# Kernel tuning notes

Measured on AMD Instinct MI355X. Metric: run time of the kernel, lower is better.

## Reference

```python
import jax, jax.numpy as jnp
import numpy as np

ALPHA_LIM = (float(np.exp(-1.0 / 5.0)), float(np.exp(-1.0 / 25.0)))
BETA_LIM = (float(np.exp(-1.0 / 30.0)), float(np.exp(-1.0 / 120.0)))
A_LIM = (-1.0, 1.0)
B_LIM = (0.0, 2.0)
THRESHOLD = 1.0


@jax.custom_vjp
def spike_boxcar(x):
    # Heaviside forward, boxcar surrogate gradient
    return (x > 0).astype(x.dtype)


def _spike_fwd(x):
    return spike_boxcar(x), x


def _spike_bwd(x, g):
    return (jnp.where(jnp.abs(x) <= 0.5, g, jnp.zeros_like(g)),)


spike_boxcar.defvjp(_spike_fwd, _spike_bwd)


def setup_inputs() -> dict:
    key = jax.random.key(0)
    ks = jax.random.split(key, 9)
    B, T, I, H = 128, 512, 512, 512
    return {
        "x": jax.random.normal(ks[0], (B, T, I), dtype=jnp.float32),
        "W": jax.random.normal(ks[1], (H, I), dtype=jnp.float32) / np.sqrt(I),
        "alpha": jax.random.uniform(ks[2], (H,), dtype=jnp.float32),
        "beta": jax.random.uniform(ks[3], (H,), dtype=jnp.float32),
        "a": jax.random.uniform(ks[4], (H,), dtype=jnp.float32),
        "b": jax.random.uniform(ks[5], (H,), dtype=jnp.float32),
        "u0": jax.random.uniform(ks[6], (B, H), dtype=jnp.float32),
        "w0": jax.random.uniform(ks[7], (B, H), dtype=jnp.float32),
        "s0": jax.random.uniform(ks[8], (B, H), dtype=jnp.float32),
    }


def reference(x, W, alpha, beta, a, b, u0, w0, s0):
    # x: [B, T, I]; W: [H, I] (nn.Linear weight, no bias)
    alpha = jnp.clip(alpha, ALPHA_LIM[0], ALPHA_LIM[1])
    beta = jnp.clip(beta, BETA_LIM[0], BETA_LIM[1])
    a = jnp.clip(a, A_LIM[0], A_LIM[1])
    b = jnp.clip(b, B_LIM[0], B_LIM[1])

    Wx = jnp.einsum("bti,hi->bth", x, W)  # [B, T, H]
    Wx_t = jnp.transpose(Wx, (1, 0, 2))    # [T, B, H] for scan over time

    def step(carry, wx_t):
        ut, wt, st = carry
        wt = beta * wt + a * ut + b * st
        ut = alpha * (ut - st) + (1.0 - alpha) * (wx_t - wt)
        st = spike_boxcar(ut - THRESHOLD)
        return (ut, wt, st), st

    _, s = jax.lax.scan(step, (u0, w0, s0), Wx_t)  # s: [T, B, H]
    return jnp.transpose(s, (1, 0, 2))  # [B, T, H]
```

## Files before the change

kernel.cpp:

```cpp
#include <hip/hip_runtime.h>
#include <hip/hip_bf16.h>


#define M_SZ 65536
#define H_SZ 512
#define K_SZ 512
#define B_SZ 128
#define T_SZ 512
#define LSTR 132

typedef __attribute__((ext_vector_type(4))) float f32x4;

__device__ __forceinline__ bool detect_bf16(const unsigned int* __restrict__ w) {
  int c = 0;
#pragma unroll
  for (int i = 0; i < 64; ++i) {
    unsigned int e = (w[i] >> 7) & 0xffu;
    c += (e >= 115u && e <= 131u) ? 1 : 0;
  }
  return c > 32;
}

template <bool ISB>
__device__ __forceinline__ f32x4 ld4t(const void* __restrict__ p, size_t off) {
  if constexpr (!ISB) {
    return *reinterpret_cast<const f32x4*>(reinterpret_cast<const float*>(p) + off);
  } else {
    uint2 v = *reinterpret_cast<const uint2*>(reinterpret_cast<const unsigned short*>(p) + off);
    f32x4 r;
    r.x = __uint_as_float((v.x & 0xffffu) << 16);
    r.y = __uint_as_float(v.x & 0xffff0000u);
    r.z = __uint_as_float((v.y & 0xffffu) << 16);
    r.w = __uint_as_float(v.y & 0xffff0000u);
    return r;
  }
}

template <bool ISB>
__device__ __forceinline__ float ld1t(const void* __restrict__ p, int i) {
  if constexpr (!ISB) return reinterpret_cast<const float*>(p)[i];
  return __uint_as_float((unsigned int)(reinterpret_cast<const unsigned short*>(p)[i]) << 16);
}

template <bool ISB>
__device__ __forceinline__ void fused_body(
    const void* __restrict__ X, const void* __restrict__ Wm,
    const void* __restrict__ alpha_p, const void* __restrict__ beta_p,
    const void* __restrict__ a_p, const void* __restrict__ b_p,
    const void* __restrict__ u0p, const void* __restrict__ w0p,
    const void* __restrict__ s0p, void* __restrict__ out,
    float* __restrict__ As, float* __restrict__ Bs, float* __restrict__ wxs) {
  const int tid = threadIdx.x;
  const int r0 = tid >> 2;
  const int q0 = (tid & 3) * 4;
  const int tx = tid & 15;
  const int ty = tid >> 4;
  const int b = blockIdx.x >> 2;
  const int N0 = (blockIdx.x & 3) * 128;

  float al = 0.f, be = 0.f, av = 0.f, bv = 0.f, om = 0.f, u = 0.f, w = 0.f, s = 0.f;
  if (tid < 128) {
    const int h = N0 + tid;
    al = fminf(fmaxf(ld1t<ISB>(alpha_p, h), (float)0.8187307530779818),
               (float)0.9607894391523232);
    be = fminf(fmaxf(ld1t<ISB>(beta_p, h), (float)0.9672161004820059),
               (float)0.9917013044213351);
    av = fminf(fmaxf(ld1t<ISB>(a_p, h), -1.0f), 1.0f);
    bv = fminf(fmaxf(ld1t<ISB>(b_p, h), 0.0f), 2.0f);
    om = __fsub_rn(1.0f, al);
    const int bh = b * H_SZ + h;
    u = ld1t<ISB>(u0p, bh);
    w = ld1t<ISB>(w0p, bh);
    s = ld1t<ISB>(s0p, bh);
  }

  float* outf = reinterpret_cast<float*>(out);
  unsigned short* outu = reinterpret_cast<unsigned short*>(out);

  for (int tt = 0; tt < 4; ++tt) {
    const size_t M0 = (size_t)b * T_SZ + tt * 128;

    float acc[8][8];
#pragma unroll
    for (int i = 0; i < 8; ++i)
#pragma unroll
      for (int j = 0; j < 8; ++j) acc[i][j] = 0.0f;

    const size_t aoff0 = (M0 + r0) * K_SZ + q0;
    const size_t aoff1 = (M0 + r0 + 64) * K_SZ + q0;
    const size_t boff0 = (size_t)(N0 + r0) * K_SZ + q0;
    const size_t boff1 = (size_t)(N0 + r0 + 64) * K_SZ + q0;

    f32x4 pa0 = ld4t<ISB>(X, aoff0), pa1 = ld4t<ISB>(X, aoff1);
    f32x4 pb0 = ld4t<ISB>(Wm, boff0), pb1 = ld4t<ISB>(Wm, boff1);

    for (int kk = 0; kk < K_SZ; kk += 16) {
      __syncthreads();
      As[(q0 + 0) * LSTR + r0] = pa0.x; As[(q0 + 1) * LSTR + r0] = pa0.y;
      As[(q0 + 2) * LSTR + r0] = pa0.z; As[(q0 + 3) * LSTR + r0] = pa0.w;
      As[(q0 + 0) * LSTR + r0 + 64] = pa1.x; As[(q0 + 1) * LSTR + r0 + 64] = pa1.y;
      As[(q0 + 2) * LSTR + r0 + 64] = pa1.z; As[(q0 + 3) * LSTR + r0 + 64] = pa1.w;
      Bs[(q0 + 0) * LSTR + r0] = pb0.x; Bs[(q0 + 1) * LSTR + r0] = pb0.y;
      Bs[(q0 + 2) * LSTR + r0] = pb0.z; Bs[(q0 + 3) * LSTR + r0] = pb0.w;
      Bs[(q0 + 0) * LSTR + r0 + 64] = pb1.x; Bs[(q0 + 1) * LSTR + r0 + 64] = pb1.y;
      Bs[(q0 + 2) * LSTR + r0 + 64] = pb1.z; Bs[(q0 + 3) * LSTR + r0 + 64] = pb1.w;
      __syncthreads();
      if (kk + 16 < K_SZ) {
        pa0 = ld4t<ISB>(X, aoff0 + kk + 16); pa1 = ld4t<ISB>(X, aoff1 + kk + 16);
        pb0 = ld4t<ISB>(Wm, boff0 + kk + 16); pb1 = ld4t<ISB>(Wm, boff1 + kk + 16);
      }
#pragma unroll
      for (int k = 0; k < 16; ++k) {
        const f32x4 a0 = *reinterpret_cast<const f32x4*>(As + k * LSTR + ty * 4);
        const f32x4 a1 = *reinterpret_cast<const f32x4*>(As + k * LSTR + 64 + ty * 4);
        const f32x4 b0 = *reinterpret_cast<const f32x4*>(Bs + k * LSTR + tx * 4);
        const f32x4 b1 = *reinterpret_cast<const f32x4*>(Bs + k * LSTR + 64 + tx * 4);
        const float avv[8] = {a0.x, a0.y, a0.z, a0.w, a1.x, a1.y, a1.z, a1.w};
        const float bvv[8] = {b0.x, b0.y, b0.z, b0.w, b1.x, b1.y, b1.z, b1.w};
#pragma unroll
        for (int i = 0; i < 8; ++i)
#pragma unroll
          for (int j = 0; j < 8; ++j) acc[i][j] += avv[i] * bvv[j];
      }
    }
#pragma unroll
    for (int sub = 0; sub < 4; ++sub) {
      __syncthreads();
      const bool owner = (sub & 1) ? (ty >= 8) : (ty < 8);
      if (owner) {
#pragma unroll
        for (int rr = 0; rr < 4; ++rr) {
          const int row = (ty & 7) * 4 + rr;
          const int r = (sub < 2) ? rr : 4 + rr;
          f32x4 v0 = {acc[r][0], acc[r][1], acc[r][2], acc[r][3]};
          f32x4 v1 = {acc[r][4], acc[r][5], acc[r][6], acc[r][7]};
          *reinterpret_cast<f32x4*>(wxs + row * 128 + tx * 4) = v0;
          *reinterpret_cast<f32x4*>(wxs + row * 128 + 64 + tx * 4) = v1;
        }
      }
      __syncthreads();
      if (tid < 128) {
        const size_t tbase =
            ((size_t)b * T_SZ + tt * 128 + sub * 32) * H_SZ + N0 + tid;
#pragma unroll
        for (int t = 0; t < 32; ++t) {
          const float cur = wxs[t * 128 + tid];
          w = __fadd_rn(__fadd_rn(__fmul_rn(be, w), __fmul_rn(av, u)), __fmul_rn(bv, s));
          u = __fadd_rn(__fmul_rn(al, __fsub_rn(u, s)), __fmul_rn(om, __fsub_rn(cur, w)));
          const bool sp = (u > 1.0f);
          s = sp ? 1.0f : 0.0f;
          if constexpr (ISB)
            outu[tbase + (size_t)t * H_SZ] = sp ? (unsigned short)0x3F80u : (unsigned short)0u;
          else
            outf[tbase + (size_t)t * H_SZ] = s;
        }
      }
    }
  }
}

__global__ __launch_bounds__(256) void adlif_fused(
    const void* __restrict__ X, const void* __restrict__ Wm,
    const void* __restrict__ alpha_p, const void* __restrict__ beta_p,
    const void* __restrict__ a_p, const void* __restrict__ b_p,
    const void* __restrict__ u0p, const void* __restrict__ w0p,
    const void* __restrict__ s0p, void* __restrict__ out) {
  __shared__ float As[16 * LSTR];
  __shared__ float Bs[16 * LSTR];
  __shared__ float wxs[32 * 128];
  if (detect_bf16(reinterpret_cast<const unsigned int*>(X)))
    fused_body<true>(X, Wm, alpha_p, beta_p, a_p, b_p, u0p, w0p, s0p, out, As, Bs, wxs);
  else
    fused_body<false>(X, Wm, alpha_p, beta_p, a_p, b_p, u0p, w0p, s0p, out, As, Bs, wxs);
}

extern "C" void kernel_launch(void* const* d_in, const int* in_sizes, int n_in,
                              void* d_out, int out_size, void* d_ws, size_t ws_size,
                              hipStream_t stream) {
  adlif_fused<<<dim3(B_SZ * 4), dim3(256), 0, stream>>>(
      d_in[0], d_in[1], d_in[2], d_in[3], d_in[4], d_in[5], d_in[6], d_in[7],
      d_in[8], d_out);
}
```

Baseline: 591.0 us.

## Double-buffer GEMM shared tiles, use nontemporal spike stores, raise occupancy hint

```diff
diff --git a/kernel.cpp b/kernel.cpp
--- a/kernel.cpp
+++ b/kernel.cpp
@@ -8,6 +8,7 @@
 #define B_SZ 128
 #define T_SZ 512
 #define LSTR 132
+#define BUFSZ (16 * LSTR)
 
 typedef __attribute__((ext_vector_type(4))) float f32x4;
 
@@ -77,6 +78,9 @@
   float* outf = reinterpret_cast<float*>(out);
   unsigned short* outu = reinterpret_cast<unsigned short*>(out);
 
+  const size_t boff0 = (size_t)(N0 + r0) * K_SZ + q0;
+  const size_t boff1 = (size_t)(N0 + r0 + 64) * K_SZ + q0;
+
   for (int tt = 0; tt < 4; ++tt) {
     const size_t M0 = (size_t)b * T_SZ + tt * 128;
 
@@ -88,33 +92,31 @@
 
     const size_t aoff0 = (M0 + r0) * K_SZ + q0;
     const size_t aoff1 = (M0 + r0 + 64) * K_SZ + q0;
-    const size_t boff0 = (size_t)(N0 + r0) * K_SZ + q0;
-    const size_t boff1 = (size_t)(N0 + r0 + 64) * K_SZ + q0;
-
-    f32x4 pa0 = ld4t<ISB>(X, aoff0), pa1 = ld4t<ISB>(X, aoff1);
-    f32x4 pb0 = ld4t<ISB>(Wm, boff0), pb1 = ld4t<ISB>(Wm, boff1);
-
-    for (int kk = 0; kk < K_SZ; kk += 16) {
-      __syncthreads();
-      As[(q0 + 0) * LSTR + r0] = pa0.x; As[(q0 + 1) * LSTR + r0] = pa0.y;
-      As[(q0 + 2) * LSTR + r0] = pa0.z; As[(q0 + 3) * LSTR + r0] = pa0.w;
-      As[(q0 + 0) * LSTR + r0 + 64] = pa1.x; As[(q0 + 1) * LSTR + r0 + 64] = pa1.y;
-      As[(q0 + 2) * LSTR + r0 + 64] = pa1.z; As[(q0 + 3) * LSTR + r0 + 64] = pa1.w;
-      Bs[(q0 + 0) * LSTR + r0] = pb0.x; Bs[(q0 + 1) * LSTR + r0] = pb0.y;
-      Bs[(q0 + 2) * LSTR + r0] = pb0.z; Bs[(q0 + 3) * LSTR + r0] = pb0.w;
-      Bs[(q0 + 0) * LSTR + r0 + 64] = pb1.x; Bs[(q0 + 1) * LSTR + r0 + 64] = pb1.y;
-      Bs[(q0 + 2) * LSTR + r0 + 64] = pb1.z; Bs[(q0 + 3) * LSTR + r0 + 64] = pb1.w;
-      __syncthreads();
-      if (kk + 16 < K_SZ) {
-        pa0 = ld4t<ISB>(X, aoff0 + kk + 16); pa1 = ld4t<ISB>(X, aoff1 + kk + 16);
-        pb0 = ld4t<ISB>(Wm, boff0 + kk + 16); pb1 = ld4t<ISB>(Wm, boff1 + kk + 16);
-      }
+
+    f32x4 pa0, pa1, pb0, pb1;
+    auto prefetch = [&](int kk) {
+      pa0 = ld4t<ISB>(X, aoff0 + kk);
+      pa1 = ld4t<ISB>(X, aoff1 + kk);
+      pb0 = ld4t<ISB>(Wm, boff0 + kk);
+      pb1 = ld4t<ISB>(Wm, boff1 + kk);
+    };
+    auto stage = [&](float* __restrict__ A, float* __restrict__ B) {
+      A[(q0 + 0) * LSTR + r0] = pa0.x; A[(q0 + 1) * LSTR + r0] = pa0.y;
+      A[(q0 + 2) * LSTR + r0] = pa0.z; A[(q0 + 3) * LSTR + r0] = pa0.w;
+      A[(q0 + 0) * LSTR + r0 + 64] = pa1.x; A[(q0 + 1) * LSTR + r0 + 64] = pa1.y;
+      A[(q0 + 2) * LSTR + r0 + 64] = pa1.z; A[(q0 + 3) * LSTR + r0 + 64] = pa1.w;
+      B[(q0 + 0) * LSTR + r0] = pb0.x; B[(q0 + 1) * LSTR + r0] = pb0.y;
+      B[(q0 + 2) * LSTR + r0] = pb0.z; B[(q0 + 3) * LSTR + r0] = pb0.w;
+      B[(q0 + 0) * LSTR + r0 + 64] = pb1.x; B[(q0 + 1) * LSTR + r0 + 64] = pb1.y;
+      B[(q0 + 2) * LSTR + r0 + 64] = pb1.z; B[(q0 + 3) * LSTR + r0 + 64] = pb1.w;
+    };
+    auto compute = [&](const float* __restrict__ A, const float* __restrict__ B) {
 #pragma unroll
       for (int k = 0; k < 16; ++k) {
-        const f32x4 a0 = *reinterpret_cast<const f32x4*>(As + k * LSTR + ty * 4);
-        const f32x4 a1 = *reinterpret_cast<const f32x4*>(As + k * LSTR + 64 + ty * 4);
-        const f32x4 b0 = *reinterpret_cast<const f32x4*>(Bs + k * LSTR + tx * 4);
-        const f32x4 b1 = *reinterpret_cast<const f32x4*>(Bs + k * LSTR + 64 + tx * 4);
+        const f32x4 a0 = *reinterpret_cast<const f32x4*>(A + k * LSTR + ty * 4);
+        const f32x4 a1 = *reinterpret_cast<const f32x4*>(A + k * LSTR + 64 + ty * 4);
+        const f32x4 b0 = *reinterpret_cast<const f32x4*>(B + k * LSTR + tx * 4);
+        const f32x4 b1 = *reinterpret_cast<const f32x4*>(B + k * LSTR + 64 + tx * 4);
         const float avv[8] = {a0.x, a0.y, a0.z, a0.w, a1.x, a1.y, a1.z, a1.w};
         const float bvv[8] = {b0.x, b0.y, b0.z, b0.w, b1.x, b1.y, b1.z, b1.w};
 #pragma unroll
@@ -122,6 +124,21 @@
 #pragma unroll
           for (int j = 0; j < 8; ++j) acc[i][j] += avv[i] * bvv[j];
       }
+    };
+
+    prefetch(0);
+    stage(As, Bs);
+    prefetch(16);
+#pragma clang loop unroll(disable)
+    for (int i = 0; i < 32; ++i) {
+      __syncthreads();
+      const int cb = (i & 1) * BUFSZ;
+      const int nb = ((i + 1) & 1) * BUFSZ;
+      if (i + 1 < 32) {
+        stage(As + nb, Bs + nb);
+        if (i + 2 < 32) prefetch(16 * (i + 2));
+      }
+      compute(As + cb, Bs + cb);
     }
 #pragma unroll
     for (int sub = 0; sub < 4; ++sub) {
@@ -150,23 +167,24 @@
           const bool sp = (u > 1.0f);
           s = sp ? 1.0f : 0.0f;
           if constexpr (ISB)
-            outu[tbase + (size_t)t * H_SZ] = sp ? (unsigned short)0x3F80u : (unsigned short)0u;
+            __builtin_nontemporal_store(sp ? (unsigned short)0x3F80u : (unsigned short)0u,
+                                        outu + tbase + (size_t)t * H_SZ);
           else
-            outf[tbase + (size_t)t * H_SZ] = s;
+            __builtin_nontemporal_store(s, outf + tbase + (size_t)t * H_SZ);
         }
       }
     }
   }
 }
 
-__global__ __launch_bounds__(256) void adlif_fused(
+__global__ __launch_bounds__(256, 2) void adlif_fused(
     const void* __restrict__ X, const void* __restrict__ Wm,
     const void* __restrict__ alpha_p, const void* __restrict__ beta_p,
     const void* __restrict__ a_p, const void* __restrict__ b_p,
     const void* __restrict__ u0p, const void* __restrict__ w0p,
     const void* __restrict__ s0p, void* __restrict__ out) {
-  __shared__ float As[16 * LSTR];
-  __shared__ float Bs[16 * LSTR];
+  __shared__ float As[2 * BUFSZ];
+  __shared__ float Bs[2 * BUFSZ];
   __shared__ float wxs[32 * 128];
   if (detect_bf16(reinterpret_cast<const unsigned int*>(X)))
     fused_body<true>(X, Wm, alpha_p, beta_p, a_p, b_p, u0p, w0p, s0p, out, As, Bs, wxs);
```

Result: slower. 833.3 us (+41.0%).
